# Performance work log

Measured on AMD Instinct MI355X. Metric: run time of the kernel, lower is better.

## Reference

```python
import jax, jax.numpy as jnp
import numpy as np

B, T, V, C, L, H = 2, 1024, 50257, 768, 12, 12
HD = C // H


def setup_inputs() -> dict:
    key = jax.random.key(0)
    ks = jax.random.split(key, 10)
    s = 0.02
    rn = lambda k, shp: (jax.random.normal(k, shp, jnp.float32) * s)
    return dict(
        idx=jax.random.randint(ks[0], (B, T), 0, V),
        wte=rn(ks[1], (V, C)),
        wpe=rn(ks[2], (T, C)),
        ln1_w=jnp.ones((L, C)), ln1_b=jnp.zeros((L, C)),
        attn_w=rn(ks[3], (L, C, 3 * C)), attn_b=jnp.zeros((L, 3 * C)),
        proj_w=rn(ks[4], (L, C, C)), proj_b=jnp.zeros((L, C)),
        ln2_w=jnp.ones((L, C)), ln2_b=jnp.zeros((L, C)),
        fc_w=rn(ks[5], (L, C, 4 * C)), fc_b=jnp.zeros((L, 4 * C)),
        fc2_w=rn(ks[6], (L, 4 * C, C)), fc2_b=jnp.zeros((L, C)),
        lnf_w=jnp.ones((C,)), lnf_b=jnp.zeros((C,)),
        lm_head_w=rn(ks[7], (V, C)),  # torch Linear layout [out, in]
    )


def _layer_norm(x, w, b):
    m = jnp.mean(x, axis=-1, keepdims=True)
    v = jnp.mean(jnp.square(x - m), axis=-1, keepdims=True)
    return (x - m) * jax.lax.rsqrt(v + 1e-5) * w + b


def reference(idx, wte, wpe, ln1_w, ln1_b, attn_w, attn_b, proj_w, proj_b,
              ln2_w, ln2_b, fc_w, fc_b, fc2_w, fc2_b, lnf_w, lnf_b, lm_head_w):
    x = wte[idx] + wpe[jnp.arange(T)]  # [B,T,C]
    mask = jnp.tril(jnp.ones((T, T), bool))

    def block(x, p):
        l1w, l1b, aw, ab, pw, pb, l2w, l2b, fw, fb, f2w, f2b = p
        h = _layer_norm(x, l1w, l1b)
        qkv = h @ aw + ab  # [B,T,3C]
        q, k, v = jnp.split(qkv, 3, axis=-1)
        split_heads = lambda t: t.reshape(B, T, H, HD).transpose(0, 2, 1, 3)
        q, k, v = split_heads(q), split_heads(k), split_heads(v)
        att = jnp.einsum('bhqd,bhkd->bhqk', q, k) * (1.0 / np.sqrt(HD))
        att = jnp.where(mask, att, -jnp.inf)
        att = jax.nn.softmax(att, axis=-1)
        y = jnp.einsum('bhqk,bhkd->bhqd', att, v)
        y = y.transpose(0, 2, 1, 3).reshape(B, T, C)
        x = x + y @ pw + pb
        h2 = _layer_norm(x, l2w, l2b)
        x = x + jax.nn.gelu(h2 @ fw + fb, approximate=True) @ f2w + f2b
        return x, None

    layer_params = (ln1_w, ln1_b, attn_w, attn_b, proj_w, proj_b,
                    ln2_w, ln2_b, fc_w, fc_b, fc2_w, fc2_b)
    x, _ = jax.lax.scan(block, x, layer_params)
    x = _layer_norm(x, lnf_w, lnf_b)
    logits = x @ lm_head_w.T  # [B,T,V]
    return logits
```

## Files before the change

kernel.cpp:

```cpp
#include <hip/hip_runtime.h>
#include <hip/hip_bf16.h>

#define Bsz 2
#define Tsz 1024
#define Vsz 50257
#define Csz 768
#define Lsz 12
#define Hsz 12
#define Msz 2048
#define VPAD 50304

typedef __attribute__((ext_vector_type(8))) short short8;
typedef __attribute__((ext_vector_type(4))) float f32x4;

__device__ __forceinline__ ushort f2bf(float f) {
  union { float f; unsigned u; } v; v.f = f;
  return (ushort)((v.u + 0x7FFFu + ((v.u >> 16) & 1u)) >> 16);
}

__device__ __forceinline__ void load_lds16(const void* g, void* l) {
  __builtin_amdgcn_global_load_lds(
      (const __attribute__((address_space(1))) unsigned int*)g,
      (__attribute__((address_space(3))) unsigned int*)l, 16, 0, 0);
}

__global__ void k_embed(const int* __restrict__ idx, const float* __restrict__ wte,
                        const float* __restrict__ wpe, float* __restrict__ x) {
  int m = blockIdx.x;
  int t = m & (Tsz - 1);
  const float* src = wte + (size_t)idx[m] * Csz;
  const float* pe  = wpe + (size_t)t * Csz;
  float* dst = x + (size_t)m * Csz;
  for (int c = threadIdx.x; c < Csz; c += 256)
    dst[c] = src[c] + pe[c];
}

__global__ void k_ln(const float* __restrict__ x, const float* __restrict__ w,
                     const float* __restrict__ b, ushort* __restrict__ out) {
  int m = blockIdx.x;
  const float* row = x + (size_t)m * Csz;
  int tid = threadIdx.x;
  float v0 = row[tid], v1 = row[tid + 256], v2 = row[tid + 512];
  float s = v0 + v1 + v2;
  float q = v0 * v0 + v1 * v1 + v2 * v2;
  for (int o = 32; o; o >>= 1) {
    s += __shfl_down(s, o, 64);
    q += __shfl_down(q, o, 64);
  }
  __shared__ float red[8];
  __shared__ float mv[2];
  int wid = tid >> 6, lane = tid & 63;
  if (!lane) { red[wid] = s; red[4 + wid] = q; }
  __syncthreads();
  if (!tid) {
    float S = red[0] + red[1] + red[2] + red[3];
    float Q = red[4] + red[5] + red[6] + red[7];
    float mean = S * (1.0f / Csz);
    float var = Q * (1.0f / Csz) - mean * mean;
    mv[0] = mean; mv[1] = rsqrtf(var + 1e-5f);
  }
  __syncthreads();
  float mean = mv[0], rs = mv[1];
  ushort* o = out + (size_t)m * Csz;
  o[tid]       = f2bf((v0 - mean) * rs * w[tid]       + b[tid]);
  o[tid + 256] = f2bf((v1 - mean) * rs * w[tid + 256] + b[tid + 256]);
  o[tid + 512] = f2bf((v2 - mean) * rs * w[tid + 512] + b[tid + 512]);
}

__global__ void k_prep(const float* __restrict__ aw, const float* __restrict__ pw,
                       const float* __restrict__ fw, const float* __restrict__ f2w,
                       ushort* __restrict__ wT, int l0, size_t lstride) {
  int t = blockIdx.x;
  int ly = l0 + blockIdx.y;
  const float* src; int R, Cn; size_t doff;
  if (t < 1728)      { src = aw  + (size_t)ly * Csz * 3 * Csz; R = Csz;     Cn = 3 * Csz; doff = 0; }
  else if (t < 2304) { t -= 1728; src = pw  + (size_t)ly * Csz * Csz;     R = Csz;     Cn = Csz;     doff = (size_t)3 * Csz * Csz; }
  else if (t < 4608) { t -= 2304; src = fw  + (size_t)ly * Csz * 4 * Csz; R = Csz;     Cn = 4 * Csz; doff = (size_t)4 * Csz * Csz; }
  else               { t -= 4608; src = f2w + (size_t)ly * 4 * Csz * Csz; R = 4 * Csz; Cn = Csz;     doff = (size_t)8 * Csz * Csz; }
  ushort* dst = wT + (size_t)blockIdx.y * lstride + doff;

  __shared__ float tb[32][33];
  int ncx = Cn / 32;
  int c0 = (t % ncx) * 32, r0 = (t / ncx) * 32;
  int tx = threadIdx.x & 31, ty = threadIdx.x >> 5;
#pragma unroll
  for (int k = 0; k < 4; k++)
    tb[ty + 8 * k][tx] = src[(size_t)(r0 + ty + 8 * k) * Cn + c0 + tx];
  __syncthreads();
#pragma unroll
  for (int k = 0; k < 4; k++)
    dst[(size_t)(c0 + ty + 8 * k) * R + r0 + tx] = f2bf(tb[tx][ty + 8 * k]);
}

__global__ void k_f32_to_bf16_pad(const float* __restrict__ src, ushort* __restrict__ dst,
                                  int n_src, int n_tot) {
  int stride = gridDim.x * 256 * 4;
  for (int i = (blockIdx.x * 256 + threadIdx.x) * 4; i < n_tot; i += stride) {
    ushort4 o;
    if (i + 3 < n_src) {
      float4 v = *(const float4*)(src + i);
      o.x = f2bf(v.x); o.y = f2bf(v.y); o.z = f2bf(v.z); o.w = f2bf(v.w);
    } else {
      o.x = o.y = o.z = o.w = 0;
    }
    *(ushort4*)(dst + i) = o;
  }
}

template <int BM, int BN, int FM, int FN, int BK, int OUT, bool SWZ, int EPI, bool NTS>
__global__ __launch_bounds__(256) void k_gemm(
    const ushort* __restrict__ A, const ushort* __restrict__ Bt,
    const float* __restrict__ bias, const float* res,
    void* __restrict__ outv, int N, int K, int ntm) {
  constexpr int RPC = (BK == 64) ? 8 : 16;
  constexpr int NCHA = BM / RPC, NCH = (BM + BN) / RPC, CPW = NCH / 4;
  constexpr int STB = 2 * (BM + BN) * BK * 2;
  constexpr int EPB = EPI ? (4 * 32 * 68 * 4) : 0;
  constexpr int SMB = STB > EPB ? STB : EPB;
  __shared__ __align__(16) char smem[SMB];

  int bid = blockIdx.x;
  if (SWZ) {
    int nwg = gridDim.x;
    bid = (bid & 7) * (nwg >> 3) + (bid >> 3);
  }
  int by = bid % ntm, bx = bid / ntm;
  int m0 = by * BM, n0 = bx * BN;

  int tid = threadIdx.x;
  int wid = tid >> 6, lane = tid & 63, lg = lane >> 4, lr = lane & 15;
  int wm = (wid >> 1) * (FM * 16), wn = (wid & 1) * (FN * 16);

  const f32x4 FZ = {0.f, 0.f, 0.f, 0.f};
  f32x4 acc[FM][FN];
#pragma unroll
  for (int i = 0; i < FM; i++)
#pragma unroll
    for (int j = 0; j < FN; j++) acc[i][j] = FZ;

  int srow, scol;
  if (BK == 64) { srow = lane >> 3; scol = ((lane & 7) ^ (srow & 7)) * 8; }
  else          { srow = lane >> 2; scol = ((lane & 3) ^ ((lane >> 3) & 3)) * 8; }

  const ushort* p[CPW];
  int ldso[CPW];
#pragma unroll
  for (int i = 0; i < CPW; i++) {
    int c = wid * CPW + i;
    ldso[i] = c * 512;
    if (c < NCHA) p[i] = A + (size_t)(m0 + c * RPC + srow) * K + scol;
    else          p[i] = Bt + (size_t)(n0 + (c - NCHA) * RPC + srow) * K + scol;
  }

  auto STAGE = [&](int buf) {
    ushort* Sb = (ushort*)smem + buf * (BM + BN) * BK;
#pragma unroll
    for (int i = 0; i < CPW; i++) {
      load_lds16(p[i], Sb + ldso[i]);
      p[i] += BK;
    }
  };
  auto COMPUTE = [&](int buf) {
    const ushort* Sb = (const ushort*)smem + buf * (BM + BN) * BK;
#pragma unroll
    for (int kk = 0; kk < BK / 32; kk++) {
      int cofs;
      if (BK == 64) cofs = (kk * 32 + lg * 8) ^ ((lr & 7) << 3);
      else          cofs = (lg * 8) ^ (((lr >> 1) & 3) << 3);
      short8 a[FM], b[FN];
#pragma unroll
      for (int f = 0; f < FM; f++)
        a[f] = *(const short8*)&Sb[(wm + f * 16 + lr) * BK + cofs];
#pragma unroll
      for (int f = 0; f < FN; f++)
        b[f] = *(const short8*)&Sb[(BM + wn + f * 16 + lr) * BK + cofs];
#pragma unroll
      for (int fi = 0; fi < FM; fi++)
#pragma unroll
        for (int fj = 0; fj < FN; fj++)
          acc[fi][fj] = __builtin_amdgcn_mfma_f32_16x16x32_bf16(a[fi], b[fj], acc[fi][fj], 0, 0, 0);
    }
  };

  int NT = K / BK;
  STAGE(0);
  __syncthreads();
  for (int t = 0;;) {
    if (t + 1 < NT) STAGE(1);
    COMPUTE(0);
    if (++t == NT) break;
    __syncthreads();
    if (t + 1 < NT) STAGE(0);
    COMPUTE(1);
    if (++t == NT) break;
    __syncthreads();
  }

  if constexpr (EPI) {
    __syncthreads();
    float* Sf = (float*)smem + wid * (32 * 68);
#pragma unroll
    for (int half = 0; half < 2; half++) {
#pragma unroll
      for (int f2 = 0; f2 < 2; f2++) {
        int fi = half * 2 + f2;
#pragma unroll
        for (int fj = 0; fj < 4; fj++)
#pragma unroll
          for (int i = 0; i < 4; i++)
            Sf[(f2 * 16 + 4 * lg + i) * 68 + fj * 16 + lr] = acc[fi][fj][i];
      }
#pragma unroll
      for (int it = 0; it < 8; it++) {
        int rl = it * 4 + lg;
        f32x4 v = *(const f32x4*)&Sf[rl * 68 + lr * 4];
        int gm = m0 + wm + half * 32 + rl;
        int gn = n0 + wn + lr * 4;
        float* op = (float*)outv + (size_t)gm * N + gn;
        if (gn + 3 < N) {
          if (NTS) __builtin_nontemporal_store(v, (f32x4*)op);
          else     *(f32x4*)op = v;
        } else {
#pragma unroll
          for (int j = 0; j < 4; j++)
            if (gn + j < N) op[j] = v[j];
        }
      }
    }
    return;
  }

#pragma unroll
  for (int fi = 0; fi < FM; fi++)
#pragma unroll
    for (int fj = 0; fj < FN; fj++) {
      int gn = n0 + wn + fj * 16 + lr;
      if (gn < N) {
        float bv = bias ? bias[gn] : 0.f;
#pragma unroll
        for (int i = 0; i < 4; i++) {
          int gm = m0 + wm + fi * 16 + 4 * lg + i;
          size_t o = (size_t)gm * N + gn;
          float v = acc[fi][fj][i] + bv;
          if (OUT == 0) {
            if (res) v += res[o];
            ((float*)outv)[o] = v;
          } else if (OUT == 1) {
            ((ushort*)outv)[o] = f2bf(v);
          } else {
            float u = 0.7978845608f * (v + 0.044715f * v * v * v);
            float t2 = __expf(2.f * u);
            float th = 1.f - 2.f / (t2 + 1.f);
            ((ushort*)outv)[o] = f2bf(0.5f * v * (1.f + th));
          }
        }
      }
    }
}

__global__ __launch_bounds__(256) void k_attn(const ushort* __restrict__ qkv,
                                              ushort* __restrict__ ybf) {
  __shared__ __align__(16) ushort Ks[64 * 72];
  __shared__ __align__(16) ushort Vs[64 * 72];
  __shared__ __align__(16) ushort Ps[4 * 16 * 72];
  int bid = blockIdx.x;
  bid = (bid & 7) * ((Bsz * Hsz * 16) >> 3) + (bid >> 3);
  int bh = bid >> 4;
  int q0 = (bid & 15) * 64;
  int b = bh / Hsz, h = bh % Hsz;
  int tid = threadIdx.x, wid = tid >> 6, lane = tid & 63, lg = lane >> 4, lr = lane & 15;
  const ushort* base = qkv + (size_t)b * Tsz * 2304;

  int qt = q0 + wid * 16 + lr;
  const ushort* qp = base + (size_t)qt * 2304 + h * 64;
  short8 aq0 = *(const short8*)(qp + lg * 8);
  short8 aq1 = *(const short8*)(qp + 32 + lg * 8);

  int srow = tid >> 3, soff = (tid & 7) * 8;
  const ushort* kp0 = base + (size_t)srow * 2304 + 768 + h * 64 + soff;
  const ushort* vp0 = kp0 + 768;
  short8 kreg[2], vreg[2];
  auto LOADKV = [&](int k0) {
#pragma unroll
    for (int r = 0; r < 2; r++) {
      kreg[r] = *(const short8*)(kp0 + (size_t)(k0 + r * 32) * 2304);
      vreg[r] = *(const short8*)(vp0 + (size_t)(k0 + r * 32) * 2304);
    }
  };
  auto WRITEKV = [&]() {
#pragma unroll
    for (int r = 0; r < 2; r++) {
      int row = srow + r * 32;
      *(short8*)&Ks[row * 72 + soff] = kreg[r];
#pragma unroll
      for (int j = 0; j < 8; j++) Vs[(soff + j) * 72 + row] = (ushort)vreg[r][j];
    }
  };

  const f32x4 FZ = {0.f, 0.f, 0.f, 0.f};
  f32x4 of[4];
  of[0] = FZ; of[1] = FZ; of[2] = FZ; of[3] = FZ;
  float mrow[4] = {-INFINITY, -INFINITY, -INFINITY, -INFINITY};
  float lrow[4] = {0.f, 0.f, 0.f, 0.f};

  int nkt = q0 / 64 + 1;
  LOADKV(0);
  for (int kt = 0; kt < nkt; kt++) {
    int k0 = kt * 64;
    WRITEKV();
    __syncthreads();
    if (kt + 1 < nkt) LOADKV(k0 + 64);

    f32x4 sf[4];
    sf[0] = FZ; sf[1] = FZ; sf[2] = FZ; sf[3] = FZ;
#pragma unroll
    for (int nf = 0; nf < 4; nf++) {
      short8 b0 = *(const short8*)&Ks[(nf * 16 + lr) * 72 + lg * 8];
      short8 b1 = *(const short8*)&Ks[(nf * 16 + lr) * 72 + 32 + lg * 8];
      sf[nf] = __builtin_amdgcn_mfma_f32_16x16x32_bf16(aq0, b0, sf[nf], 0, 0, 0);
      sf[nf] = __builtin_amdgcn_mfma_f32_16x16x32_bf16(aq1, b1, sf[nf], 0, 0, 0);
    }

    bool last = (kt == nkt - 1);
#pragma unroll
    for (int i = 0; i < 4; i++) {
      int qr = q0 + wid * 16 + 4 * lg + i;
      float s[4];
#pragma unroll
      for (int nf = 0; nf < 4; nf++) {
        s[nf] = sf[nf][i] * 0.125f;
        if (last && k0 + nf * 16 + lr > qr) s[nf] = -INFINITY;
      }
      float rm = fmaxf(fmaxf(s[0], s[1]), fmaxf(s[2], s[3]));
#pragma unroll
      for (int o = 1; o < 16; o <<= 1) rm = fmaxf(rm, __shfl_xor(rm, o, 16));
      float mnew = fmaxf(mrow[i], rm);
      float scale = __expf(mrow[i] - mnew);
      float rs = 0.f;
#pragma unroll
      for (int nf = 0; nf < 4; nf++) {
        float p = __expf(s[nf] - mnew);
        rs += p;
        Ps[(wid * 16 + 4 * lg + i) * 72 + nf * 16 + lr] = f2bf(p);
      }
#pragma unroll
      for (int o = 1; o < 16; o <<= 1) rs += __shfl_xor(rs, o, 16);
      lrow[i] = lrow[i] * scale + rs;
      mrow[i] = mnew;
      of[0][i] *= scale; of[1][i] *= scale; of[2][i] *= scale; of[3][i] *= scale;
    }
    __syncthreads();

    short8 ap0 = *(const short8*)&Ps[(wid * 16 + lr) * 72 + lg * 8];
    short8 ap1 = *(const short8*)&Ps[(wid * 16 + lr) * 72 + 32 + lg * 8];
#pragma unroll
    for (int df = 0; df < 4; df++) {
      short8 bv0 = *(const short8*)&Vs[(df * 16 + lr) * 72 + lg * 8];
      short8 bv1 = *(const short8*)&Vs[(df * 16 + lr) * 72 + 32 + lg * 8];
      of[df] = __builtin_amdgcn_mfma_f32_16x16x32_bf16(ap0, bv0, of[df], 0, 0, 0);
      of[df] = __builtin_amdgcn_mfma_f32_16x16x32_bf16(ap1, bv1, of[df], 0, 0, 0);
    }
    __syncthreads();
  }

  ushort* yp = ybf + (size_t)b * Tsz * Csz;
#pragma unroll
  for (int df = 0; df < 4; df++)
#pragma unroll
    for (int i = 0; i < 4; i++) {
      int qr = q0 + wid * 16 + 4 * lg + i;
      float v = of[df][i] / lrow[i];
      yp[(size_t)qr * Csz + h * 64 + df * 16 + lr] = f2bf(v);
    }
}

extern "C" void kernel_launch(void* const* d_in, const int* in_sizes, int n_in,
                              void* d_out, int out_size, void* d_ws, size_t ws_size,
                              hipStream_t stream) {
  (void)in_sizes; (void)n_in; (void)out_size;
  const int* idx      = (const int*)d_in[0];
  const float* wte    = (const float*)d_in[1];
  const float* wpe    = (const float*)d_in[2];
  const float* ln1_w  = (const float*)d_in[3];
  const float* ln1_b  = (const float*)d_in[4];
  const float* attn_w = (const float*)d_in[5];
  const float* attn_b = (const float*)d_in[6];
  const float* proj_w = (const float*)d_in[7];
  const float* proj_b = (const float*)d_in[8];
  const float* ln2_w  = (const float*)d_in[9];
  const float* ln2_b  = (const float*)d_in[10];
  const float* fc_w   = (const float*)d_in[11];
  const float* fc_b   = (const float*)d_in[12];
  const float* fc2_w  = (const float*)d_in[13];
  const float* fc2_b  = (const float*)d_in[14];
  const float* lnf_w  = (const float*)d_in[15];
  const float* lnf_b  = (const float*)d_in[16];
  const float* lm_w   = (const float*)d_in[17];
  float* out = (float*)d_out;

  char* ws = (char*)d_ws;
  float*  x     = (float*)(ws + 0);
  ushort* qkvbf = (ushort*)(ws + 6291456);
  ushort* abuf  = (ushort*)(ws + 15728640);
  ushort* hbuf  = (ushort*)(ws + 18874368);
  ushort* lmw   = (ushort*)(ws + 31457280);
  ushort* wT    = (ushort*)(ws + 108724224);
  const size_t LSTRIDE = (size_t)12 * Csz * Csz;
  const size_t NEED_FULL = 108724224ull + LSTRIDE * 2 * Lsz;
  bool full = ws_size >= NEED_FULL;

  k_embed<<<Msz, 256, 0, stream>>>(idx, wte, wpe, x);
  k_f32_to_bf16_pad<<<4096, 256, 0, stream>>>(lm_w, lmw, Vsz * Csz, VPAD * Csz);
  if (full)
    k_prep<<<dim3(6912, Lsz), 256, 0, stream>>>(attn_w, proj_w, fc_w, fc2_w, wT, 0, LSTRIDE);

  for (int l = 0; l < Lsz; l++) {
    ushort* wTl = wT + (full ? (size_t)l * LSTRIDE : 0);
    if (!full)
      k_prep<<<dim3(6912, 1), 256, 0, stream>>>(attn_w, proj_w, fc_w, fc2_w, wTl, l, 0);
    const ushort* qkvW = wTl;
    const ushort* projW = wTl + (size_t)3 * Csz * Csz;
    const ushort* fcW   = wTl + (size_t)4 * Csz * Csz;
    const ushort* fc2W  = wTl + (size_t)8 * Csz * Csz;

    k_ln<<<Msz, 256, 0, stream>>>(x, ln1_w + l * Csz, ln1_b + l * Csz, abuf);
    k_gemm<128, 96, 4, 3, 64, 1, false, 0, false><<<(Msz / 128) * (3 * Csz / 96), 256, 0, stream>>>(
        abuf, qkvW, attn_b + (size_t)l * 3 * Csz, nullptr, qkvbf, 3 * Csz, Csz, Msz / 128);
    k_attn<<<Bsz * Hsz * 16, 256, 0, stream>>>(qkvbf, abuf);
    k_gemm<64, 96, 2, 3, 64, 0, false, 0, false><<<(Msz / 64) * (Csz / 96), 256, 0, stream>>>(
        abuf, projW, proj_b + (size_t)l * Csz, x, x, Csz, Csz, Msz / 64);
    k_ln<<<Msz, 256, 0, stream>>>(x, ln2_w + l * Csz, ln2_b + l * Csz, abuf);
    k_gemm<128, 128, 4, 4, 64, 2, false, 0, false><<<(Msz / 128) * (4 * Csz / 128), 256, 0, stream>>>(
        abuf, fcW, fc_b + (size_t)l * 4 * Csz, nullptr, hbuf, 4 * Csz, Csz, Msz / 128);
    k_gemm<64, 96, 2, 3, 64, 0, false, 0, false><<<(Msz / 64) * (Csz / 96), 256, 0, stream>>>(
        hbuf, fc2W, fc2_b + (size_t)l * Csz, x, x, Csz, 4 * Csz, Msz / 64);
  }

  k_ln<<<Msz, 256, 0, stream>>>(x, lnf_w, lnf_b, abuf);
  int ntm = Msz / 128;
  k_gemm<128, 128, 4, 4, 32, 0, true, 1, true><<<ntm * (VPAD / 128), 256, 0, stream>>>(
      abuf, lmw, nullptr, nullptr, out, Vsz, Csz, ntm);
}
```

Before: 2.438 ms.

## Widen attention KV tile to 128, use warp-per-row layernorm, drop nontemporal stores

Attention now handles 128 keys per iteration, which halves the loop trips and barriers, widens the V and P shared-memory tiles, and doubles the registers used for K/V prefetch. LayerNorm maps one wavefront to each row, reducing with xor-shuffles and no shared memory or block barriers, and launches a quarter as many blocks. The LM-head epilogue goes back to normal stores instead of nontemporal stores. The causal masking on the last tile now does more wasted work for query blocks that only partly fill a 128-key tile, and the extra registers may lower occupancy.

```diff
diff --git a/kernel.cpp b/kernel.cpp
--- a/kernel.cpp
+++ b/kernel.cpp
@@ -37,34 +37,30 @@
 
 __global__ void k_ln(const float* __restrict__ x, const float* __restrict__ w,
                      const float* __restrict__ b, ushort* __restrict__ out) {
-  int m = blockIdx.x;
-  const float* row = x + (size_t)m * Csz;
-  int tid = threadIdx.x;
-  float v0 = row[tid], v1 = row[tid + 256], v2 = row[tid + 512];
-  float s = v0 + v1 + v2;
-  float q = v0 * v0 + v1 * v1 + v2 * v2;
-  for (int o = 32; o; o >>= 1) {
-    s += __shfl_down(s, o, 64);
-    q += __shfl_down(q, o, 64);
-  }
-  __shared__ float red[8];
-  __shared__ float mv[2];
-  int wid = tid >> 6, lane = tid & 63;
-  if (!lane) { red[wid] = s; red[4 + wid] = q; }
-  __syncthreads();
-  if (!tid) {
-    float S = red[0] + red[1] + red[2] + red[3];
-    float Q = red[4] + red[5] + red[6] + red[7];
-    float mean = S * (1.0f / Csz);
-    float var = Q * (1.0f / Csz) - mean * mean;
-    mv[0] = mean; mv[1] = rsqrtf(var + 1e-5f);
-  }
-  __syncthreads();
-  float mean = mv[0], rs = mv[1];
-  ushort* o = out + (size_t)m * Csz;
-  o[tid]       = f2bf((v0 - mean) * rs * w[tid]       + b[tid]);
-  o[tid + 256] = f2bf((v1 - mean) * rs * w[tid + 256] + b[tid + 256]);
-  o[tid + 512] = f2bf((v2 - mean) * rs * w[tid + 512] + b[tid + 512]);
+  int r = blockIdx.x * 4 + (threadIdx.x >> 6);
+  int lane = threadIdx.x & 63;
+  const float* row = x + (size_t)r * Csz;
+  float v[12];
+  float s = 0.f, q = 0.f;
+#pragma unroll
+  for (int j = 0; j < 12; j++) {
+    v[j] = row[lane + j * 64];
+    s += v[j];
+    q += v[j] * v[j];
+  }
+#pragma unroll
+  for (int o = 1; o < 64; o <<= 1) {
+    s += __shfl_xor(s, o, 64);
+    q += __shfl_xor(q, o, 64);
+  }
+  float mean = s * (1.0f / Csz);
+  float rstd = rsqrtf(q * (1.0f / Csz) - mean * mean + 1e-5f);
+  ushort* o = out + (size_t)r * Csz;
+#pragma unroll
+  for (int j = 0; j < 12; j++) {
+    int c = lane + j * 64;
+    o[c] = f2bf((v[j] - mean) * rstd * w[c] + b[c]);
+  }
 }
 
 __global__ void k_prep(const float* __restrict__ aw, const float* __restrict__ pw,
@@ -107,7 +103,7 @@
   }
 }
 
-template <int BM, int BN, int FM, int FN, int BK, int OUT, bool SWZ, int EPI, bool NTS>
+template <int BM, int BN, int FM, int FN, int BK, int OUT, bool SWZ, int EPI>
 __global__ __launch_bounds__(256) void k_gemm(
     const ushort* __restrict__ A, const ushort* __restrict__ Bt,
     const float* __restrict__ bias, const float* res,
@@ -218,8 +214,7 @@
         int gn = n0 + wn + lr * 4;
         float* op = (float*)outv + (size_t)gm * N + gn;
         if (gn + 3 < N) {
-          if (NTS) __builtin_nontemporal_store(v, (f32x4*)op);
-          else     *(f32x4*)op = v;
+          *(f32x4*)op = v;
         } else {
 #pragma unroll
           for (int j = 0; j < 4; j++)
@@ -260,9 +255,9 @@
 
 __global__ __launch_bounds__(256) void k_attn(const ushort* __restrict__ qkv,
                                               ushort* __restrict__ ybf) {
-  __shared__ __align__(16) ushort Ks[64 * 72];
-  __shared__ __align__(16) ushort Vs[64 * 72];
-  __shared__ __align__(16) ushort Ps[4 * 16 * 72];
+  __shared__ __align__(16) ushort Ks[128 * 72];
+  __shared__ __align__(16) ushort Vs[64 * 136];
+  __shared__ __align__(16) ushort Ps[4 * 16 * 136];
   int bid = blockIdx.x;
   bid = (bid & 7) * ((Bsz * Hsz * 16) >> 3) + (bid >> 3);
   int bh = bid >> 4;
@@ -279,21 +274,21 @@
   int srow = tid >> 3, soff = (tid & 7) * 8;
   const ushort* kp0 = base + (size_t)srow * 2304 + 768 + h * 64 + soff;
   const ushort* vp0 = kp0 + 768;
-  short8 kreg[2], vreg[2];
+  short8 kreg[4], vreg[4];
   auto LOADKV = [&](int k0) {
 #pragma unroll
-    for (int r = 0; r < 2; r++) {
+    for (int r = 0; r < 4; r++) {
       kreg[r] = *(const short8*)(kp0 + (size_t)(k0 + r * 32) * 2304);
       vreg[r] = *(const short8*)(vp0 + (size_t)(k0 + r * 32) * 2304);
     }
   };
   auto WRITEKV = [&]() {
 #pragma unroll
-    for (int r = 0; r < 2; r++) {
+    for (int r = 0; r < 4; r++) {
       int row = srow + r * 32;
       *(short8*)&Ks[row * 72 + soff] = kreg[r];
 #pragma unroll
-      for (int j = 0; j < 8; j++) Vs[(soff + j) * 72 + row] = (ushort)vreg[r][j];
+      for (int j = 0; j < 8; j++) Vs[(soff + j) * 136 + row] = (ushort)vreg[r][j];
     }
   };
 
@@ -303,18 +298,18 @@
   float mrow[4] = {-INFINITY, -INFINITY, -INFINITY, -INFINITY};
   float lrow[4] = {0.f, 0.f, 0.f, 0.f};
 
-  int nkt = q0 / 64 + 1;
+  int nkt = (q0 >> 7) + 1;
   LOADKV(0);
   for (int kt = 0; kt < nkt; kt++) {
-    int k0 = kt * 64;
+    int k0 = kt * 128;
     WRITEKV();
     __syncthreads();
-    if (kt + 1 < nkt) LOADKV(k0 + 64);
-
-    f32x4 sf[4];
-    sf[0] = FZ; sf[1] = FZ; sf[2] = FZ; sf[3] = FZ;
-#pragma unroll
-    for (int nf = 0; nf < 4; nf++) {
+    if (kt + 1 < nkt) LOADKV(k0 + 128);
+
+    f32x4 sf[8];
+#pragma unroll
+    for (int nf = 0; nf < 8; nf++) {
+      sf[nf] = FZ;
       short8 b0 = *(const short8*)&Ks[(nf * 16 + lr) * 72 + lg * 8];
       short8 b1 = *(const short8*)&Ks[(nf * 16 + lr) * 72 + 32 + lg * 8];
       sf[nf] = __builtin_amdgcn_mfma_f32_16x16x32_bf16(aq0, b0, sf[nf], 0, 0, 0);
@@ -325,23 +320,25 @@
 #pragma unroll
     for (int i = 0; i < 4; i++) {
       int qr = q0 + wid * 16 + 4 * lg + i;
-      float s[4];
-#pragma unroll
-      for (int nf = 0; nf < 4; nf++) {
+      float s[8];
+#pragma unroll
+      for (int nf = 0; nf < 8; nf++) {
         s[nf] = sf[nf][i] * 0.125f;
         if (last && k0 + nf * 16 + lr > qr) s[nf] = -INFINITY;
       }
-      float rm = fmaxf(fmaxf(s[0], s[1]), fmaxf(s[2], s[3]));
+      float rm = s[0];
+#pragma unroll
+      for (int nf = 1; nf < 8; nf++) rm = fmaxf(rm, s[nf]);
 #pragma unroll
       for (int o = 1; o < 16; o <<= 1) rm = fmaxf(rm, __shfl_xor(rm, o, 16));
       float mnew = fmaxf(mrow[i], rm);
       float scale = __expf(mrow[i] - mnew);
       float rs = 0.f;
 #pragma unroll
-      for (int nf = 0; nf < 4; nf++) {
+      for (int nf = 0; nf < 8; nf++) {
         float p = __expf(s[nf] - mnew);
         rs += p;
-        Ps[(wid * 16 + 4 * lg + i) * 72 + nf * 16 + lr] = f2bf(p);
+        Ps[(wid * 16 + 4 * lg + i) * 136 + nf * 16 + lr] = f2bf(p);
       }
 #pragma unroll
       for (int o = 1; o < 16; o <<= 1) rs += __shfl_xor(rs, o, 16);
@@ -351,14 +348,17 @@
     }
     __syncthreads();
 
-    short8 ap0 = *(const short8*)&Ps[(wid * 16 + lr) * 72 + lg * 8];
-    short8 ap1 = *(const short8*)&Ps[(wid * 16 + lr) * 72 + 32 + lg * 8];
+    short8 ap[4];
+#pragma unroll
+    for (int c = 0; c < 4; c++)
+      ap[c] = *(const short8*)&Ps[(wid * 16 + lr) * 136 + c * 32 + lg * 8];
 #pragma unroll
     for (int df = 0; df < 4; df++) {
-      short8 bv0 = *(const short8*)&Vs[(df * 16 + lr) * 72 + lg * 8];
-      short8 bv1 = *(const short8*)&Vs[(df * 16 + lr) * 72 + 32 + lg * 8];
-      of[df] = __builtin_amdgcn_mfma_f32_16x16x32_bf16(ap0, bv0, of[df], 0, 0, 0);
-      of[df] = __builtin_amdgcn_mfma_f32_16x16x32_bf16(ap1, bv1, of[df], 0, 0, 0);
+#pragma unroll
+      for (int c = 0; c < 4; c++) {
+        short8 bv = *(const short8*)&Vs[(df * 16 + lr) * 136 + c * 32 + lg * 8];
+        of[df] = __builtin_amdgcn_mfma_f32_16x16x32_bf16(ap[c], bv, of[df], 0, 0, 0);
+      }
     }
     __syncthreads();
   }
@@ -423,21 +423,21 @@
     const ushort* fcW   = wTl + (size_t)4 * Csz * Csz;
     const ushort* fc2W  = wTl + (size_t)8 * Csz * Csz;
 
-    k_ln<<<Msz, 256, 0, stream>>>(x, ln1_w + l * Csz, ln1_b + l * Csz, abuf);
-    k_gemm<128, 96, 4, 3, 64, 1, false, 0, false><<<(Msz / 128) * (3 * Csz / 96), 256, 0, stream>>>(
+    k_ln<<<Msz / 4, 256, 0, stream>>>(x, ln1_w + l * Csz, ln1_b + l * Csz, abuf);
+    k_gemm<128, 96, 4, 3, 64, 1, false, 0><<<(Msz / 128) * (3 * Csz / 96), 256, 0, stream>>>(
         abuf, qkvW, attn_b + (size_t)l * 3 * Csz, nullptr, qkvbf, 3 * Csz, Csz, Msz / 128);
     k_attn<<<Bsz * Hsz * 16, 256, 0, stream>>>(qkvbf, abuf);
-    k_gemm<64, 96, 2, 3, 64, 0, false, 0, false><<<(Msz / 64) * (Csz / 96), 256, 0, stream>>>(
+    k_gemm<64, 96, 2, 3, 64, 0, false, 0><<<(Msz / 64) * (Csz / 96), 256, 0, stream>>>(
         abuf, projW, proj_b + (size_t)l * Csz, x, x, Csz, Csz, Msz / 64);
-    k_ln<<<Msz, 256, 0, stream>>>(x, ln2_w + l * Csz, ln2_b + l * Csz, abuf);
-    k_gemm<128, 128, 4, 4, 64, 2, false, 0, false><<<(Msz / 128) * (4 * Csz / 128), 256, 0, stream>>>(
+    k_ln<<<Msz / 4, 256, 0, stream>>>(x, ln2_w + l * Csz, ln2_b + l * Csz, abuf);
+    k_gemm<128, 128, 4, 4, 64, 2, false, 0><<<(Msz / 128) * (4 * Csz / 128), 256, 0, stream>>>(
         abuf, fcW, fc_b + (size_t)l * 4 * Csz, nullptr, hbuf, 4 * Csz, Csz, Msz / 128);
-    k_gemm<64, 96, 2, 3, 64, 0, false, 0, false><<<(Msz / 64) * (Csz / 96), 256, 0, stream>>>(
+    k_gemm<64, 96, 2, 3, 64, 0, false, 0><<<(Msz / 64) * (Csz / 96), 256, 0, stream>>>(
         hbuf, fc2W, fc2_b + (size_t)l * Csz, x, x, Csz, 4 * Csz, Msz / 64);
   }
 
-  k_ln<<<Msz, 256, 0, stream>>>(x, lnf_w, lnf_b, abuf);
+  k_ln<<<Msz / 4, 256, 0, stream>>>(x, lnf_w, lnf_b, abuf);
   int ntm = Msz / 128;
-  k_gemm<128, 128, 4, 4, 32, 0, true, 1, true><<<ntm * (VPAD / 128), 256, 0, stream>>>(
+  k_gemm<128, 128, 4, 4, 32, 0, true, 1><<<ntm * (VPAD / 128), 256, 0, stream>>>(
       abuf, lmw, nullptr, nullptr, out, Vsz, Csz, ntm);
 }
```

Measured after the change: 2.385 ms. 2.2% less time.
